# Kernel tuning notes

Measured on AMD Instinct MI355X. Metric: run time of the kernel, lower is better.

The kernel has to match this reference:

```python
import jax, jax.numpy as jnp
import numpy as np

HIDDEN = 1280
NUM_HEADS = 16
NUM_KV_HEADS = 4
HEAD_DIM = 80
Q_SIZE = NUM_HEADS * HEAD_DIM          # 1280
KV_SIZE = NUM_KV_HEADS * HEAD_DIM      # 320
QKV_OUT = Q_SIZE + 2 * KV_SIZE         # 1920
R_SOFTPLUS_0 = 1.442695041


def setup_inputs() -> dict:
    key = jax.random.key(0)
    ks = jax.random.split(key, 6)
    B, S = 4, 2048
    return {
        "hidden_states": jax.random.normal(ks[0], (B, S, HIDDEN), dtype=jnp.float32),
        "scaling": jax.random.normal(ks[1], (HEAD_DIM,), dtype=jnp.float32),
        "qkv_w": jax.random.normal(ks[2], (QKV_OUT, HIDDEN), dtype=jnp.float32) * (1.0 / np.sqrt(HIDDEN)),
        "qkv_b": jax.random.normal(ks[3], (QKV_OUT,), dtype=jnp.float32) * 0.01,
        "o_w": jax.random.normal(ks[4], (HIDDEN, Q_SIZE), dtype=jnp.float32) * (1.0 / np.sqrt(Q_SIZE)),
        "o_b": jax.random.normal(ks[5], (HIDDEN,), dtype=jnp.float32) * 0.01,
    }


def reference(hidden_states, scaling, qkv_w, qkv_b, o_w, o_b):
    B, S, _ = hidden_states.shape
    qkv = hidden_states @ qkv_w.T + qkv_b                      # [B,S,1920]
    xq = qkv[..., :Q_SIZE].reshape(B, S, NUM_HEADS, HEAD_DIM)
    xk = qkv[..., Q_SIZE:Q_SIZE + KV_SIZE].reshape(B, S, NUM_KV_HEADS, HEAD_DIM)
    xv = qkv[..., Q_SIZE + KV_SIZE:].reshape(B, S, NUM_KV_HEADS, HEAD_DIM)
    # learned per-head-dim scaling: (r_softplus_0/sqrt(d)) * softplus(scaling)
    scale = (R_SOFTPLUS_0 / np.sqrt(HEAD_DIM)) * jax.nn.softplus(scaling)
    xq = xq * scale[None, None, None, :]
    # GQA: expand kv heads to match query heads (repeat_interleave on head dim)
    nq_per_kv = NUM_HEADS // NUM_KV_HEADS
    k = jnp.repeat(xk, nq_per_kv, axis=2)                      # [B,S,H,d]
    v = jnp.repeat(xv, nq_per_kv, axis=2)
    scores = jnp.einsum("bqhd,bkhd->bhqk", xq, k)              # [B,H,S,S]
    probs = jax.nn.softmax(scores.astype(jnp.float32), axis=-1).astype(xq.dtype)
    out = jnp.einsum("bhqk,bkhd->bqhd", probs, v)              # [B,S,H,d]
    out = out.reshape(B, S, Q_SIZE)
    return out @ o_w.T + o_b
```

## Files before the change

kernel.cpp:

```cpp
#include <hip/hip_runtime.h>

#define HIDDEN 1280
#define QOUT   1920
#define QSIZE  1280
#define KVSIZE 320
#define NHEAD  16
#define NKV    4
#define DH     80
#define SEQ    2048
#define BATCH  4
#define MTOT   (BATCH * SEQ)
#define NT64   (SEQ / 64)
#define KTILE_ELEMS 6144
#define VTILE_ELEMS 5120

typedef __attribute__((ext_vector_type(8))) short bf16x8;
typedef __attribute__((ext_vector_type(4))) short bf16x4;
typedef __attribute__((ext_vector_type(4))) float f32x4;

__device__ __forceinline__ unsigned short f2bf(float x) {
  union { float f; unsigned u; } v; v.f = x;
  unsigned r = v.u + 0x7fffu + ((v.u >> 16) & 1u);
  return (unsigned short)(r >> 16);
}

__device__ __forceinline__ unsigned packbf(float a, float b) {
  union { float f; unsigned u; } ua, ub;
  ua.f = a; ub.f = b;
  return __builtin_amdgcn_perm(ub.u + 0x8000u, ua.u + 0x8000u, 0x07060302u);
}

__device__ __forceinline__ unsigned packbf_t(float a, float b) {
  union { float f; unsigned u; } ua, ub;
  ua.f = a; ub.f = b;
  return __builtin_amdgcn_perm(ub.u, ua.u, 0x07060302u);
}

__device__ __forceinline__ float exp2x(float x) {
#if __has_builtin(__builtin_amdgcn_exp2f)
  return __builtin_amdgcn_exp2f(x);
#else
  return exp2f(x);
#endif
}

__device__ __forceinline__ void async_copy16(const void* g, void* lds) {
  __builtin_amdgcn_global_load_lds(
      (const __attribute__((address_space(1))) unsigned int*)g,
      (__attribute__((address_space(3))) unsigned int*)lds, 16, 0, 0);
}

#define HSB   (MTOT * HIDDEN / 4 / 256)
#define QWB   (QOUT * HIDDEN / 4 / 256)
#define OWB   (HIDDEN * QSIZE / 4 / 256)
__global__ __launch_bounds__(256) void prep_k(const float* __restrict__ hs,
                                              const float* __restrict__ qkv_w,
                                              const float* __restrict__ o_w,
                                              const float* __restrict__ scaling,
                                              unsigned short* __restrict__ hs_bf,
                                              unsigned short* __restrict__ qkvw_bf,
                                              unsigned short* __restrict__ ow_bf,
                                              float* __restrict__ cs) {
  const int bid = blockIdx.x, tid = threadIdx.x;
  const float* src; unsigned short* dst; int i;
  if (bid < HSB)            { src = hs;    dst = hs_bf;   i = bid * 256 + tid; }
  else if (bid < HSB + QWB) { src = qkv_w; dst = qkvw_bf; i = (bid - HSB) * 256 + tid; }
  else if (bid < HSB + QWB + OWB) { src = o_w; dst = ow_bf; i = (bid - HSB - QWB) * 256 + tid; }
  else {
    int n = (bid - HSB - QWB - OWB) * 256 + tid;
    if (n < QOUT) {
      float v = 1.0f;
      if (n < QSIZE) {
        float x = scaling[n % DH];
        float sp = (x > 20.f) ? x : log1pf(__expf(x));
        v = 1.442695041f * 1.442695041f * 0.11180339887f * sp;
      }
      cs[n] = v;
    }
    return;
  }
  float4 v = ((const float4*)src)[i];
  ushort4 o;
  o.x = f2bf(v.x); o.y = f2bf(v.y); o.z = f2bf(v.z); o.w = f2bf(v.w);
  ((ushort4*)dst)[i] = o;
}

template <bool OUT_BF16, bool USE_SCALE>
__global__ __launch_bounds__(512) void gemm_bt(const unsigned short* __restrict__ A,
                                               const unsigned short* __restrict__ Bt,
                                               const float* __restrict__ bias,
                                               const float* __restrict__ colscale,
                                               void* __restrict__ Cout,
                                               int M, int N, int K) {
  __shared__ unsigned short As[256 * 64];
  __shared__ unsigned short Bs[128 * 64];
  const int tid  = threadIdx.x;
  const int wave = tid >> 6, lane = tid & 63;
  const int r = lane & 15, quad = lane >> 4;
  const int xm = r & 7;
  const int gx = gridDim.x;
  int lid = blockIdx.y * gx + blockIdx.x;
  const int cpx = (gx * gridDim.y) >> 3;
  lid = (lid & 7) * cpx + (lid >> 3);
  const int m0 = (lid / gx) * 256, n0 = (lid % gx) * 128;
  const int rm = (wave >> 1) * 64, cn = (wave & 1) * 64;

  f32x4 acc[4][4];
#pragma unroll
  for (int i = 0; i < 4; ++i)
#pragma unroll
    for (int j = 0; j < 4; ++j) acc[i][j] = f32x4{0.f, 0.f, 0.f, 0.f};

  for (int k0 = 0; k0 < K; k0 += 64) {
    __syncthreads();
#pragma unroll
    for (int j = 0; j < 4; ++j) {
      const int c = tid + j * 512;
      const int row = c >> 3, sp = c & 7;
      const int sd = (sp ^ (row & 7)) * 8;
      async_copy16(A + (size_t)(m0 + row) * K + k0 + sd, &As[c * 8]);
    }
#pragma unroll
    for (int j = 0; j < 2; ++j) {
      const int c = tid + j * 512;
      const int row = c >> 3, sp = c & 7;
      const int sd = (sp ^ (row & 7)) * 8;
      async_copy16(Bt + (size_t)(n0 + row) * K + k0 + sd, &Bs[c * 8]);
    }
    __syncthreads();
#pragma unroll
    for (int kk = 0; kk < 2; ++kk) {
      bf16x8 af[4], bfr[4];
#pragma unroll
      for (int mi = 0; mi < 4; ++mi)
        af[mi] = *(const bf16x8*)&As[(rm + mi * 16 + r) * 64 + ((kk * 4 + quad) ^ xm) * 8];
#pragma unroll
      for (int ni = 0; ni < 4; ++ni)
        bfr[ni] = *(const bf16x8*)&Bs[(cn + ni * 16 + r) * 64 + ((kk * 4 + quad) ^ xm) * 8];
#pragma unroll
      for (int mi = 0; mi < 4; ++mi)
#pragma unroll
        for (int ni = 0; ni < 4; ++ni)
          acc[mi][ni] = __builtin_amdgcn_mfma_f32_16x16x32_bf16(af[mi], bfr[ni], acc[mi][ni], 0, 0, 0);
    }
  }

#pragma unroll
  for (int ni = 0; ni < 4; ++ni) {
    const int n = n0 + cn + ni * 16 + r;
    const float bn = bias[n];
    const float sc = USE_SCALE ? colscale[n] : 1.0f;
#pragma unroll
    for (int mi = 0; mi < 4; ++mi) {
#pragma unroll
      for (int reg = 0; reg < 4; ++reg) {
        const int m = m0 + rm + mi * 16 + quad * 4 + reg;
        const float v = (acc[mi][ni][reg] + bn) * sc;
        if (OUT_BF16)
          ((unsigned short*)Cout)[(size_t)m * N + n] = f2bf(v);
        else
          ((float*)Cout)[(size_t)m * N + n] = v;
      }
    }
  }
}

__global__ __launch_bounds__(256) void kvpack(const unsigned short* __restrict__ qkv,
                                              unsigned short* __restrict__ Kp,
                                              unsigned short* __restrict__ Vp) {
  const int st = blockIdx.x, kvh = blockIdx.y, b = blockIdx.z;
  const int tid = threadIdx.x;
  unsigned short* kout = Kp + (size_t)((b * NKV + kvh) * NT64 + st) * KTILE_ELEMS;
#pragma unroll
  for (int j = 0; j < 3; ++j) {
    int c = tid + j * 256;
    int row = c / 12, cir = c - row * 12;
    int kk = cir >> 2, sp = cir & 3;
    int sd = sp ^ ((row >> 1) & 3);
    int d0 = kk * 32 + sd * 8;
    int skey = (row >> 5) * 32 + ((row >> 2) & 3) * 8 + ((row >> 4) & 1) * 4 + (row & 3);
    uint4 v = {0, 0, 0, 0};
    if (d0 < DH)
      v = *(const uint4*)&qkv[(size_t)(b * SEQ + st * 64 + skey) * QOUT +
                              QSIZE + kvh * DH + d0];
    *(uint4*)&kout[row * 96 + kk * 32 + sp * 8] = v;
  }
  __shared__ unsigned short tile[64][88];
  for (int c = tid; c < 640; c += 256) {
    int row = c / 10, seg = c % 10;
    uint4 v = *(const uint4*)&qkv[(size_t)(b * SEQ + st * 64 + row) * QOUT +
                                  QSIZE + KVSIZE + kvh * DH + seg * 8];
    *(uint4*)&tile[row][seg * 8] = v;
  }
  __syncthreads();
  unsigned short* vout = Vp + (size_t)((b * NKV + kvh) * NT64 + st) * VTILE_ELEMS;
  for (int c = tid; c < 5120; c += 256) {
    int d = c >> 6, key = c & 63;
    vout[d * 64 + (key ^ ((d & 7) << 3))] = tile[key][d];
  }
}

__global__ __launch_bounds__(512, 4) void attn(const unsigned short* __restrict__ qkv,
                                               const unsigned short* __restrict__ Kp,
                                               const unsigned short* __restrict__ Vp,
                                               unsigned short* __restrict__ att) {
  int qt, h, b;
  {
    int lid = (blockIdx.z * 16 + blockIdx.y) * 8 + blockIdx.x;
    lid = (lid & 7) * 64 + (lid >> 3);
    qt = lid & 7; h = (lid >> 3) & 15; b = lid >> 7;
  }
  const int kvh = h >> 2;
  const int tid = threadIdx.x;
  const int wave = tid >> 6, lane = tid & 63;
  const int r = lane & 15, quad = lane >> 4;
  const int sq8 = (quad ^ ((r >> 1) & 3)) * 8;

  __shared__ unsigned short Ks[2][64 * 96];
  __shared__ unsigned short Vs[2][96 * 64];

  {
    const uint4 ones = {0x3F803F80u, 0x3F803F80u, 0x3F803F80u, 0x3F803F80u};
    for (int c = tid; c < 256; c += 512)
      *(uint4*)&Vs[c >> 7][80 * 64 + (c & 127) * 8] = ones;
  }

  const int qbase = qt * 256 + wave * 32;
  bf16x8 qb[2][3];
#pragma unroll
  for (int t = 0; t < 2; ++t)
#pragma unroll
    for (int kk = 0; kk < 3; ++kk)
      qb[t][kk] = *(const bf16x8*)&qkv[(size_t)(b * SEQ + qbase + t * 16 + r) * QOUT +
                                       h * DH + kk * 32 + quad * 8];

  f32x4 o_acc[6][2];
#pragma unroll
  for (int i = 0; i < 6; ++i)
#pragma unroll
    for (int t = 0; t < 2; ++t) o_acc[i][t] = f32x4{0.f, 0.f, 0.f, 0.f};

  const unsigned short* kp = Kp + (size_t)((b * NKV + kvh) * NT64) * KTILE_ELEMS;
  const unsigned short* vp = Vp + (size_t)((b * NKV + kvh) * NT64) * VTILE_ELEMS;

#define STAGE(bufi, kt_) do {                                                   \
    const unsigned short* kpt = kp + (size_t)(kt_) * KTILE_ELEMS;               \
    async_copy16(kpt + tid * 8, &Ks[bufi][tid * 8]);                            \
    if (tid < 256) async_copy16(kpt + (tid + 512) * 8, &Ks[bufi][(tid + 512) * 8]); \
    const unsigned short* vpt = vp + (size_t)(kt_) * VTILE_ELEMS;               \
    async_copy16(vpt + tid * 8, &Vs[bufi][tid * 8]);                            \
    if (tid < 128) async_copy16(vpt + (tid + 512) * 8, &Vs[bufi][(tid + 512) * 8]); \
  } while (0)

  STAGE(0, 0);
  __syncthreads();

  for (int kt = 0; kt < NT64; ++kt) {
    const int cur = kt & 1;
    if (kt + 1 < NT64) STAGE(cur ^ 1, kt + 1);

    f32x4 s[2][2][2];
    __builtin_amdgcn_s_setprio(1);
#pragma unroll
    for (int ntp = 0; ntp < 2; ++ntp)
#pragma unroll
      for (int half = 0; half < 2; ++half) {
        bf16x8 ka[3];
#pragma unroll
        for (int kk = 0; kk < 3; ++kk)
          ka[kk] = *(const bf16x8*)&Ks[cur][(ntp * 32 + half * 16 + r) * 96 + kk * 32 + sq8];
#pragma unroll
        for (int t = 0; t < 2; ++t) {
          f32x4 a0 = f32x4{0.f, 0.f, 0.f, 0.f};
#pragma unroll
          for (int kk = 0; kk < 3; ++kk)
            a0 = __builtin_amdgcn_mfma_f32_16x16x32_bf16(ka[kk], qb[t][kk], a0, 0, 0, 0);
          s[ntp][half][t] = a0;
        }
      }
    __builtin_amdgcn_s_setprio(0);

#pragma unroll
    for (int ntp = 0; ntp < 2; ++ntp) {
      uint4 pw[2];
#pragma unroll
      for (int t = 0; t < 2; ++t) {
        pw[t].x = packbf_t(exp2x(s[ntp][0][t][0]), exp2x(s[ntp][0][t][1]));
        pw[t].y = packbf_t(exp2x(s[ntp][0][t][2]), exp2x(s[ntp][0][t][3]));
        pw[t].z = packbf_t(exp2x(s[ntp][1][t][0]), exp2x(s[ntp][1][t][1]));
        pw[t].w = packbf_t(exp2x(s[ntp][1][t][2]), exp2x(s[ntp][1][t][3]));
      }
      __builtin_amdgcn_s_setprio(1);
#pragma unroll
      for (int nt2 = 0; nt2 < 6; ++nt2) {
        bf16x8 va = *(const bf16x8*)&Vs[cur][(nt2 * 16 + r) * 64 +
                                             (((ntp * 4 + quad) ^ (r & 7)) << 3)];
#pragma unroll
        for (int t = 0; t < 2; ++t) {
          union { uint4 u; bf16x8 v; } pv; pv.u = pw[t];
          o_acc[nt2][t] = __builtin_amdgcn_mfma_f32_16x16x32_bf16(va, pv.v, o_acc[nt2][t], 0, 0, 0);
        }
      }
      __builtin_amdgcn_s_setprio(0);
    }
    __syncthreads();
  }
#undef STAGE

#pragma unroll
  for (int t = 0; t < 2; ++t) {
    const float il = 1.0f / o_acc[5][t][0];
    const size_t q = (size_t)(b * SEQ + qbase + t * 16 + r);
#pragma unroll
    for (int nt2 = 0; nt2 < 5; ++nt2) {
      uint2 w;
      w.x = packbf(o_acc[nt2][t][0] * il, o_acc[nt2][t][1] * il);
      w.y = packbf(o_acc[nt2][t][2] * il, o_acc[nt2][t][3] * il);
      *(uint2*)&att[q * QSIZE + h * DH + nt2 * 16 + quad * 4] = w;
    }
  }
}

extern "C" void kernel_launch(void* const* d_in, const int* in_sizes, int n_in,
                              void* d_out, int out_size, void* d_ws, size_t ws_size,
                              hipStream_t stream) {
  const float* hs      = (const float*)d_in[0];
  const float* scaling = (const float*)d_in[1];
  const float* qkv_w   = (const float*)d_in[2];
  const float* qkv_b   = (const float*)d_in[3];
  const float* o_w     = (const float*)d_in[4];
  const float* o_b     = (const float*)d_in[5];

  char* p = (char*)d_ws;
  unsigned short* hs_bf   = (unsigned short*)p; p += (size_t)MTOT * HIDDEN * 2;
  unsigned short* qkvw_bf = (unsigned short*)p; p += (size_t)QOUT * HIDDEN * 2;
  unsigned short* ow_bf   = (unsigned short*)p; p += (size_t)HIDDEN * QSIZE * 2;
  float* cscale           = (float*)p;          p += (size_t)QOUT * 4;
  unsigned short* qkv     = (unsigned short*)p; p += (size_t)MTOT * QOUT * 2;
  unsigned short* Kp      = (unsigned short*)p; p += (size_t)BATCH * NKV * NT64 * KTILE_ELEMS * 2;
  unsigned short* Vp      = (unsigned short*)p; p += (size_t)BATCH * NKV * NT64 * VTILE_ELEMS * 2;
  unsigned short* att     = hs_bf;

  prep_k<<<HSB + QWB + OWB + 8, 256, 0, stream>>>(hs, qkv_w, o_w, scaling,
                                                  hs_bf, qkvw_bf, ow_bf, cscale);

  dim3 g1(QOUT / 128, MTOT / 256);
  gemm_bt<true, true><<<g1, 512, 0, stream>>>(hs_bf, qkvw_bf, qkv_b, cscale, qkv,
                                              MTOT, QOUT, HIDDEN);
  dim3 gp(NT64, NKV, BATCH);
  kvpack<<<gp, 256, 0, stream>>>(qkv, Kp, Vp);
  dim3 g3(SEQ / 256, NHEAD, BATCH);
  attn<<<g3, 512, 0, stream>>>(qkv, Kp, Vp, att);
  dim3 g4(QSIZE / 128, MTOT / 256);
  gemm_bt<false, false><<<g4, 512, 0, stream>>>(att, ow_bf, o_b, nullptr, d_out,
                                                MTOT, QSIZE, HIDDEN);
}
```

Before: 275.0 us.

## Fuse K/V tile packing into QKV GEMM epilogue and drop kvpack kernel

The QKV projection GEMM epilogue now writes K and V columns straight into the swizzled tiled Kp/Vp layouts the attention kernel expects, and the separate kvpack kernel is removed. This cuts a kernel launch and the re-read of K/V from the qkv buffer. The cost is scattered 2-byte stores in the epilogue, which may coalesce poorly. The Q load offsets in attention are adjusted so the padded 80-to-96 dim chunk no longer reads past Q's columns into K data that is no longer written to qkv.

```diff
diff --git a/kernel.cpp b/kernel.cpp
--- a/kernel.cpp
+++ b/kernel.cpp
@@ -85,12 +85,14 @@
   ((ushort4*)dst)[i] = o;
 }
 
-template <bool OUT_BF16, bool USE_SCALE>
+template <bool OUT_BF16, bool USE_SCALE, bool PACK_KV>
 __global__ __launch_bounds__(512) void gemm_bt(const unsigned short* __restrict__ A,
                                                const unsigned short* __restrict__ Bt,
                                                const float* __restrict__ bias,
                                                const float* __restrict__ colscale,
                                                void* __restrict__ Cout,
+                                               unsigned short* __restrict__ Kp,
+                                               unsigned short* __restrict__ Vp,
                                                int M, int N, int K) {
   __shared__ unsigned short As[256 * 64];
   __shared__ unsigned short Bs[128 * 64];
@@ -148,6 +150,7 @@
 #pragma unroll
   for (int ni = 0; ni < 4; ++ni) {
     const int n = n0 + cn + ni * 16 + r;
+    const int nbase = n0 + cn + ni * 16;
     const float bn = bias[n];
     const float sc = USE_SCALE ? colscale[n] : 1.0f;
 #pragma unroll
@@ -156,47 +159,35 @@
       for (int reg = 0; reg < 4; ++reg) {
         const int m = m0 + rm + mi * 16 + quad * 4 + reg;
         const float v = (acc[mi][ni][reg] + bn) * sc;
-        if (OUT_BF16)
-          ((unsigned short*)Cout)[(size_t)m * N + n] = f2bf(v);
-        else
-          ((float*)Cout)[(size_t)m * N + n] = v;
-      }
-    }
-  }
-}
-
-__global__ __launch_bounds__(256) void kvpack(const unsigned short* __restrict__ qkv,
-                                              unsigned short* __restrict__ Kp,
-                                              unsigned short* __restrict__ Vp) {
-  const int st = blockIdx.x, kvh = blockIdx.y, b = blockIdx.z;
-  const int tid = threadIdx.x;
-  unsigned short* kout = Kp + (size_t)((b * NKV + kvh) * NT64 + st) * KTILE_ELEMS;
-#pragma unroll
-  for (int j = 0; j < 3; ++j) {
-    int c = tid + j * 256;
-    int row = c / 12, cir = c - row * 12;
-    int kk = cir >> 2, sp = cir & 3;
-    int sd = sp ^ ((row >> 1) & 3);
-    int d0 = kk * 32 + sd * 8;
-    int skey = (row >> 5) * 32 + ((row >> 2) & 3) * 8 + ((row >> 4) & 1) * 4 + (row & 3);
-    uint4 v = {0, 0, 0, 0};
-    if (d0 < DH)
-      v = *(const uint4*)&qkv[(size_t)(b * SEQ + st * 64 + skey) * QOUT +
-                              QSIZE + kvh * DH + d0];
-    *(uint4*)&kout[row * 96 + kk * 32 + sp * 8] = v;
-  }
-  __shared__ unsigned short tile[64][88];
-  for (int c = tid; c < 640; c += 256) {
-    int row = c / 10, seg = c % 10;
-    uint4 v = *(const uint4*)&qkv[(size_t)(b * SEQ + st * 64 + row) * QOUT +
-                                  QSIZE + KVSIZE + kvh * DH + seg * 8];
-    *(uint4*)&tile[row][seg * 8] = v;
-  }
-  __syncthreads();
-  unsigned short* vout = Vp + (size_t)((b * NKV + kvh) * NT64 + st) * VTILE_ELEMS;
-  for (int c = tid; c < 5120; c += 256) {
-    int d = c >> 6, key = c & 63;
-    vout[d * 64 + (key ^ ((d & 7) << 3))] = tile[key][d];
+        const unsigned short bv = f2bf(v);
+        if (!PACK_KV || nbase < QSIZE) {
+          if (OUT_BF16)
+            ((unsigned short*)Cout)[(size_t)m * N + n] = bv;
+          else
+            ((float*)Cout)[(size_t)m * N + n] = v;
+        } else {
+          const int b = m >> 11, seq = m & 2047;
+          const int st = seq >> 6, key = seq & 63;
+          if (nbase < QSIZE + KVSIZE) {
+            const int c = n - QSIZE;
+            const int kvh = c / DH, d = c - kvh * DH;
+            const int row = ((key >> 5) << 5) + (((key >> 2) & 1) << 4) +
+                            (((key >> 3) & 3) << 2) + (key & 3);
+            const int sw = (row >> 1) & 3;
+            unsigned short* kt = Kp + (size_t)((b * NKV + kvh) * NT64 + st) * KTILE_ELEMS +
+                                 row * 96;
+            kt[(d >> 5) * 32 + ((((d >> 3) & 3) ^ sw) << 3) + (d & 7)] = bv;
+            if (d >= 64)
+              kt[64 + (((((d >> 3) & 3) ^ 2) ^ sw) << 3) + (d & 7)] = 0;
+          } else {
+            const int c = n - (QSIZE + KVSIZE);
+            const int kvh = c / DH, d = c - kvh * DH;
+            Vp[(size_t)((b * NKV + kvh) * NT64 + st) * VTILE_ELEMS +
+               d * 64 + (key ^ ((d & 7) << 3))] = bv;
+          }
+        }
+      }
+    }
   }
 }
 
@@ -230,9 +221,12 @@
 #pragma unroll
   for (int t = 0; t < 2; ++t)
 #pragma unroll
-    for (int kk = 0; kk < 3; ++kk)
+    for (int kk = 0; kk < 3; ++kk) {
+      int off = kk * 32 + quad * 8;
+      if (kk == 2 && quad >= 2) off -= 32;
       qb[t][kk] = *(const bf16x8*)&qkv[(size_t)(b * SEQ + qbase + t * 16 + r) * QOUT +
-                                       h * DH + kk * 32 + quad * 8];
+                                       h * DH + off];
+    }
 
   f32x4 o_acc[6][2];
 #pragma unroll
@@ -345,13 +339,11 @@
                                                   hs_bf, qkvw_bf, ow_bf, cscale);
 
   dim3 g1(QOUT / 128, MTOT / 256);
-  gemm_bt<true, true><<<g1, 512, 0, stream>>>(hs_bf, qkvw_bf, qkv_b, cscale, qkv,
-                                              MTOT, QOUT, HIDDEN);
-  dim3 gp(NT64, NKV, BATCH);
-  kvpack<<<gp, 256, 0, stream>>>(qkv, Kp, Vp);
+  gemm_bt<true, true, true><<<g1, 512, 0, stream>>>(hs_bf, qkvw_bf, qkv_b, cscale, qkv,
+                                                    Kp, Vp, MTOT, QOUT, HIDDEN);
   dim3 g3(SEQ / 256, NHEAD, BATCH);
   attn<<<g3, 512, 0, stream>>>(qkv, Kp, Vp, att);
   dim3 g4(QSIZE / 128, MTOT / 256);
-  gemm_bt<false, false><<<g4, 512, 0, stream>>>(att, ow_bf, o_b, nullptr, d_out,
-                                                MTOT, QSIZE, HIDDEN);
-}
+  gemm_bt<false, false, false><<<g4, 512, 0, stream>>>(att, ow_bf, o_b, nullptr, d_out,
+                                                       nullptr, nullptr, MTOT, QSIZE, HIDDEN);
+}
```

Result: slower. 284.0 us (+3.3%).
